# Optimization experiments

Measured on AMD Instinct MI355X. Metric: run time of the kernel, lower is better.

Reference implementation:

```python
import jax, jax.numpy as jnp
import numpy as np

B, DIN, DOUT, GRID_SIZE, SPLINE_ORDER, N_LAYERS = 4096, 1024, 1024, 8, 3, 2
COEFFS = GRID_SIZE + SPLINE_ORDER  # 11


def _kaiming_uniform(key, shape, fan_in):
    # torch nn.init.kaiming_uniform_ default: a=0 -> gain=sqrt(2), bound=sqrt(3)*gain/sqrt(fan_in)
    bound = float(np.sqrt(6.0 / fan_in))
    return jax.random.uniform(key, shape, jnp.float32, -bound, bound)


def setup_inputs() -> dict:
    key = jax.random.key(0)
    ks = jax.random.split(key, 1 + 3 * N_LAYERS)
    x = jax.random.normal(ks[0], (B, DIN), dtype=jnp.float32)
    # knot grid: arange(-so, gs+so+1)*h + lo, h=(hi-lo)/gs  -> shape [GRID_SIZE+2*SPLINE_ORDER+1]
    h = 2.0 / GRID_SIZE
    grid = jnp.arange(-SPLINE_ORDER, GRID_SIZE + SPLINE_ORDER + 1, dtype=jnp.float32) * h - 1.0
    base_w, spline_w, scaler = [], [], []
    for i in range(N_LAYERS):
        base_w.append(_kaiming_uniform(ks[1 + 3 * i], (DOUT, DIN), DIN))
        spline_w.append(_kaiming_uniform(ks[2 + 3 * i], (DOUT, DIN, COEFFS), DIN * COEFFS))
        scaler.append(_kaiming_uniform(ks[3 + 3 * i], (DOUT, DIN), DIN))
    return {
        "x": x,
        "base_w": jnp.stack(base_w),      # [L, DOUT, DIN]
        "spline_w": jnp.stack(spline_w),  # [L, DOUT, DIN, COEFFS]
        "scaler": jnp.stack(scaler),      # [L, DOUT, DIN]
        "grid": grid,                      # [G]
        "spline_order": SPLINE_ORDER,
    }


def b_splines(x, grid, spline_order):
    # x: (B, DIN) -> bases: (B, DIN, COEFFS) via Cox-de Boor recursion
    x = x[..., None]  # (B, DIN, 1)
    bases = ((x >= grid[:-1]) & (x < grid[1:])).astype(x.dtype)  # order-0 indicators
    for k in range(1, spline_order + 1):
        left = (x - grid[: -(k + 1)]) / (grid[k:-1] - grid[: -(k + 1)])
        right = (grid[k + 1:] - x) / (grid[k + 1:] - grid[1:-k])
        bases = left * bases[..., :-1] + right * bases[..., 1:]
    return bases


def reference(x, base_w, spline_w, scaler, grid, spline_order):
    so = int(spline_order)
    n_layers = base_w.shape[0]
    for i in range(n_layers):
        x = jax.nn.silu(x)                                  # base_activation applied before both branches
        base_out = x @ base_w[i].T                          # (B, DOUT)
        bs = b_splines(x, grid, so)                         # (B, DIN, COEFFS)
        w = spline_w[i] * scaler[i][..., None]              # (DOUT, DIN, COEFFS)
        spline_out = jnp.einsum("bic,oic->bo", bs, w)      # == F.linear on flattened (DIN*COEFFS)
        x = base_out + spline_out
    return x
```

## Files before the change

### kernel.cpp

```cpp
#include <hip/hip_runtime.h>
#include <stdint.h>

#define BATCH 4096
#define DIN 1024
#define DOUT 1024
#define NC 11
#define KD 12288
#define NKNOTS 15

typedef __bf16 bf16x8 __attribute__((ext_vector_type(8)));
typedef float f32x4 __attribute__((ext_vector_type(4)));

__device__ __forceinline__ unsigned short f2bf(float f) {
    unsigned int u = __float_as_uint(f);
    unsigned int r = (u + 0x7FFFu + ((u >> 16) & 1u)) >> 16;
    return (unsigned short)r;
}

__global__ __launch_bounds__(256) void build_A(
    const float* __restrict__ x, const float* __restrict__ P, int np,
    const float* __restrict__ grid, unsigned short* __restrict__ A) {
    __shared__ __align__(16) unsigned short lbs[256 * NC];
    const int tid = threadIdx.x;
    const int b  = blockIdx.x >> 2;
    const int i0 = (blockIdx.x & 3) * 256;
    const int i  = i0 + tid;

    float g[NKNOTS];
#pragma unroll
    for (int j = 0; j < NKNOTS; ++j) g[j] = grid[j];

    float xv = x[(size_t)b * DIN + i];
    for (int p = 0; p < np; ++p)
        xv += P[(size_t)p * BATCH * DIN + (size_t)b * DIN + i];
    const float s = xv / (1.f + __expf(-xv));

    float bs[14];
#pragma unroll
    for (int c = 0; c < 14; ++c) bs[c] = (s >= g[c] && s < g[c + 1]) ? 1.f : 0.f;
#pragma unroll
    for (int k = 1; k <= 3; ++k) {
        const float inv = (k == 1) ? 4.f : (k == 2) ? 2.f : (4.f / 3.f);
#pragma unroll
        for (int c = 0; c < 14 - k; ++c) {
            float left  = (s - g[c]) * inv;
            float right = (g[c + k + 1] - s) * inv;
            bs[c] = left * bs[c] + right * bs[c + 1];
        }
    }

    A[(size_t)b * KD + i] = f2bf(s);
#pragma unroll
    for (int c = 0; c < NC; ++c) lbs[tid * NC + c] = f2bf(bs[c]);
    __syncthreads();

    const uint4* src = (const uint4*)lbs;
    uint4* dst = (uint4*)(A + (size_t)b * KD + DIN + (size_t)i0 * NC);
    for (int j = tid; j < 352; j += 256) dst[j] = src[j];
}

__global__ __launch_bounds__(256) void build_W(
    const float* __restrict__ base_w, const float* __restrict__ spline_w,
    const float* __restrict__ scaler, unsigned short* __restrict__ W) {
    __shared__ __align__(16) unsigned short lw[256 * NC];
    const int tid = threadIdx.x;
    const int o  = blockIdx.x >> 2;
    const int i0 = (blockIdx.x & 3) * 256;
    const int i  = i0 + tid;
    const size_t oi = (size_t)o * DIN + i;

    const float sc = scaler[oi];
    W[(size_t)o * KD + i] = f2bf(base_w[oi]);
    const float* sw = spline_w + oi * NC;
#pragma unroll
    for (int c = 0; c < NC; ++c) lw[tid * NC + c] = f2bf(sw[c] * sc);
    __syncthreads();

    const uint4* src = (const uint4*)lw;
    uint4* dst = (uint4*)(W + (size_t)o * KD + DIN + (size_t)i0 * NC);
    for (int j = tid; j < 352; j += 256) dst[j] = src[j];
}

#define BM 256
#define BN 256
#define BK 64

#define LOADAF(AF, BASE)                                                       \
    _Pragma("unroll")                                                          \
    for (int fm = 0; fm < 4; ++fm)                                             \
        _Pragma("unroll")                                                      \
        for (int ks = 0; ks < 2; ++ks)                                         \
            AF[fm][ks] = *(const bf16x8*)&(BASE)[(wm * 64 + fm * 16 + rof) * 64 + \
                                                 (((ks * 4 + kcol) ^ xr) * 8)];

#define LOADBF(BF, BASE)                                                       \
    _Pragma("unroll")                                                          \
    for (int fn = 0; fn < 2; ++fn)                                             \
        _Pragma("unroll")                                                      \
        for (int ks = 0; ks < 2; ++ks)                                         \
            BF[fn][ks] = *(const bf16x8*)&(BASE)[(wn * 32 + fn * 16 + rof) * 64 + \
                                                 (((ks * 4 + kcol) ^ xr) * 8)];

#define MFMA16(AF, BF, RO, CO)                                                 \
    __builtin_amdgcn_s_setprio(1);                                             \
    _Pragma("unroll")                                                          \
    for (int ks = 0; ks < 2; ++ks)                                             \
        _Pragma("unroll")                                                      \
        for (int fm = 0; fm < 4; ++fm)                                         \
            _Pragma("unroll")                                                  \
            for (int fn = 0; fn < 2; ++fn)                                     \
                acc[(RO) + fm][(CO) + fn] =                                    \
                    __builtin_amdgcn_mfma_f32_16x16x32_bf16(                   \
                        AF[fm][ks], BF[fn][ks], acc[(RO) + fm][(CO) + fn], 0, 0, 0); \
    __builtin_amdgcn_s_setprio(0);

#define SBAR  __builtin_amdgcn_s_barrier()
#define SCHED __builtin_amdgcn_sched_barrier(0)

__global__ __launch_bounds__(512, 2) void gemm_kan(
    const unsigned short* __restrict__ A,
    const unsigned short* __restrict__ W,
    float* __restrict__ C, float* __restrict__ Part,
    int kspl, int ktper) {
    __shared__ unsigned short As[2 * 2 * 8192];
    __shared__ unsigned short Bs[2 * 2 * 8192];

    const int tid  = threadIdx.x;
    const int wave = tid >> 6;
    const int lane = tid & 63;
    const int per = 16 * kspl;
    const int n0  = (blockIdx.x / per) * BN;
    const int r   = blockIdx.x % per;
    const int ksp = r % kspl;
    const int m0  = (r / kspl) * BM;
    const int wm = wave >> 2;
    const int wn = wave & 3;

    const int srow = lane >> 3;
    const int scol = 8 * ((lane & 7) ^ (lane >> 3));
    const int kbase = ksp * ktper * BK;

    f32x4 acc[8][4];
#pragma unroll
    for (int a = 0; a < 8; ++a)
#pragma unroll
        for (int b = 0; b < 4; ++b) acc[a][b] = (f32x4){0.f, 0.f, 0.f, 0.f};

    auto stageA = [&](int buf, int h, int kt) {
        const int kk = kbase + kt * BK + scol;
#pragma unroll
        for (int c = 0; c < 2; ++c) {
            const int chunk = wave * 2 + c;
            const unsigned short* ga =
                A + (size_t)(m0 + h * 128 + chunk * 8 + srow) * KD + kk;
            __builtin_amdgcn_global_load_lds(
                (const __attribute__((address_space(1))) unsigned int*)ga,
                (__attribute__((address_space(3))) unsigned int*)
                    &As[buf * 16384 + h * 8192 + chunk * 512], 16, 0, 0);
        }
    };
    auto stageB = [&](int buf, int h, int kt) {
        const int kk = kbase + kt * BK + scol;
#pragma unroll
        for (int c = 0; c < 2; ++c) {
            const int chunk = wave * 2 + c;
            const unsigned short* gb =
                W + (size_t)(n0 + h * 128 + chunk * 8 + srow) * KD + kk;
            __builtin_amdgcn_global_load_lds(
                (const __attribute__((address_space(1))) unsigned int*)gb,
                (__attribute__((address_space(3))) unsigned int*)
                    &Bs[buf * 16384 + h * 8192 + chunk * 512], 16, 0, 0);
        }
    };

    stageB(0, 0, 0); stageB(0, 1, 0); stageA(0, 0, 0); stageA(0, 1, 0);
    asm volatile("s_waitcnt vmcnt(2)" ::: "memory");
    SBAR;

    const int rof  = lane & 15;
    const int xr   = lane & 7;
    const int kcol = lane >> 4;

    bf16x8 af[4][2], b0[2][2], b1[2][2];

    for (int t = 0; t < ktper; ++t) {
        const int cur = t & 1;
        const int nxt = cur ^ 1;
        const bool pf = (t + 1 < ktper);
        const unsigned short* Ab = &As[cur * 16384];
        const unsigned short* Bb = &Bs[cur * 16384];

        LOADAF(af, Ab);
        LOADBF(b0, Bb);
        if (pf) stageB(nxt, 0, t + 1);
        asm volatile("s_waitcnt lgkmcnt(8)" ::: "memory");
        SBAR;
        asm volatile("s_waitcnt lgkmcnt(0)" ::: "memory");
        SCHED;
        MFMA16(af, b0, 0, 0);
        SCHED;
        SBAR;

        LOADBF(b1, Bb + 8192);
        if (pf) stageB(nxt, 1, t + 1);
        SBAR;
        asm volatile("s_waitcnt lgkmcnt(0)" ::: "memory");
        SCHED;
        MFMA16(af, b1, 0, 2);
        SCHED;
        if (pf) { asm volatile("s_waitcnt vmcnt(4)" ::: "memory"); }
        else    { asm volatile("s_waitcnt vmcnt(0)" ::: "memory"); }
        SBAR;

        LOADAF(af, Ab + 8192);
        if (pf) stageA(nxt, 0, t + 1);
        SBAR;
        asm volatile("s_waitcnt lgkmcnt(0)" ::: "memory");
        SCHED;
        MFMA16(af, b1, 4, 2);
        SCHED;
        SBAR;

        if (pf) stageA(nxt, 1, t + 1);
        SBAR;
        SCHED;
        MFMA16(af, b0, 4, 0);
        SCHED;
        if (pf) { asm volatile("s_waitcnt vmcnt(2)" ::: "memory"); }
        SBAR;
    }

    float* Cp = (ksp == 0) ? C : (Part + (size_t)(ksp - 1) * BATCH * DOUT);
    const int crow = (lane >> 4) * 4;
    const int ccol = lane & 15;
#pragma unroll
    for (int H = 0; H < 2; ++H)
#pragma unroll
        for (int fm = 0; fm < 4; ++fm)
#pragma unroll
            for (int F = 0; F < 2; ++F)
#pragma unroll
                for (int fn = 0; fn < 2; ++fn) {
                    const int row = m0 + H * 128 + wm * 64 + fm * 16 + crow;
                    const int col = n0 + F * 128 + wn * 32 + fn * 16 + ccol;
#pragma unroll
                    for (int rr = 0; rr < 4; ++rr)
                        Cp[(size_t)(row + rr) * DOUT + col] =
                            acc[H * 4 + fm][F * 2 + fn][rr];
                }
}

__global__ __launch_bounds__(256) void reduce_add(
    const float* __restrict__ P, float* __restrict__ X, int np) {
    const size_t i = ((size_t)blockIdx.x * 256 + threadIdx.x) * 4;
    f32x4 a = *(const f32x4*)(X + i);
    for (int p = 0; p < np; ++p)
        a = a + *(const f32x4*)(P + (size_t)p * BATCH * DOUT + i);
    *(f32x4*)(X + i) = a;
}

extern "C" void kernel_launch(void* const* d_in, const int* in_sizes, int n_in,
                              void* d_out, int out_size, void* d_ws, size_t ws_size,
                              hipStream_t stream) {
    const float* x        = (const float*)d_in[0];
    const float* base_w   = (const float*)d_in[1];
    const float* spline_w = (const float*)d_in[2];
    const float* scaler   = (const float*)d_in[3];
    const float* grid     = (const float*)d_in[4];
    float* out = (float*)d_out;

    char* ws = (char*)d_ws;
    unsigned short* Abf = (unsigned short*)ws;
    unsigned short* Wbf = (unsigned short*)(ws + 100663296);
    float* xtmp = (float*)(ws + 100663296 + 25165824);
    float* Part = (float*)(ws + 100663296 + 25165824 + 16777216);

    const size_t base_need = 100663296u + 25165824u + 16777216u;
    const int kspl = (ws_size >= base_need + 3u * 16777216u) ? 4 : 2;
    const int ktper = (KD / BK) / kspl;

    for (int layer = 0; layer < 2; ++layer) {
        const float* xin = (layer == 0) ? x : xtmp;
        float* xout      = (layer == 0) ? xtmp : out;
        build_W<<<4096, 256, 0, stream>>>(base_w + (size_t)layer * DOUT * DIN,
                                          spline_w + (size_t)layer * DOUT * DIN * NC,
                                          scaler + (size_t)layer * DOUT * DIN, Wbf);
        build_A<<<16384, 256, 0, stream>>>(xin, Part, (layer == 0) ? 0 : kspl - 1,
                                           grid, Abf);
        gemm_kan<<<64 * kspl, 512, 0, stream>>>(Abf, Wbf, xout, Part, kspl, ktper);
    }
    reduce_add<<<BATCH * DOUT / 1024, 256, 0, stream>>>(Part, out, kspl - 1);
}
```

Measured before the change: 293.7 us.

## Replace split-K partial buffers and reduction with atomic adds into output

```diff
diff --git a/kernel.cpp b/kernel.cpp
--- a/kernel.cpp
+++ b/kernel.cpp
@@ -18,8 +18,8 @@
 }
 
 __global__ __launch_bounds__(256) void build_A(
-    const float* __restrict__ x, const float* __restrict__ P, int np,
-    const float* __restrict__ grid, unsigned short* __restrict__ A) {
+    const float* __restrict__ x, const float* __restrict__ grid,
+    unsigned short* __restrict__ A) {
     __shared__ __align__(16) unsigned short lbs[256 * NC];
     const int tid = threadIdx.x;
     const int b  = blockIdx.x >> 2;
@@ -30,10 +30,8 @@
 #pragma unroll
     for (int j = 0; j < NKNOTS; ++j) g[j] = grid[j];
 
-    float xv = x[(size_t)b * DIN + i];
-    for (int p = 0; p < np; ++p)
-        xv += P[(size_t)p * BATCH * DIN + (size_t)b * DIN + i];
-    const float s = xv / (1.f + __expf(-xv));
+    const float xv = x[(size_t)b * DIN + i];
+    const float s  = xv / (1.f + __expf(-xv));
 
     float bs[14];
 #pragma unroll
@@ -84,6 +82,8 @@
 #define BM 256
 #define BN 256
 #define BK 64
+#define KSPL 4
+#define KTPER 48
 
 #define LOADAF(AF, BASE)                                                       \
     _Pragma("unroll")                                                          \
@@ -120,25 +120,24 @@
 __global__ __launch_bounds__(512, 2) void gemm_kan(
     const unsigned short* __restrict__ A,
     const unsigned short* __restrict__ W,
-    float* __restrict__ C, float* __restrict__ Part,
-    int kspl, int ktper) {
+    float* __restrict__ Out) {
     __shared__ unsigned short As[2 * 2 * 8192];
     __shared__ unsigned short Bs[2 * 2 * 8192];
 
     const int tid  = threadIdx.x;
     const int wave = tid >> 6;
     const int lane = tid & 63;
-    const int per = 16 * kspl;
+    const int per = 16 * KSPL;
     const int n0  = (blockIdx.x / per) * BN;
     const int r   = blockIdx.x % per;
-    const int ksp = r % kspl;
-    const int m0  = (r / kspl) * BM;
+    const int ksp = r % KSPL;
+    const int m0  = (r / KSPL) * BM;
     const int wm = wave >> 2;
     const int wn = wave & 3;
 
     const int srow = lane >> 3;
     const int scol = 8 * ((lane & 7) ^ (lane >> 3));
-    const int kbase = ksp * ktper * BK;
+    const int kbase = ksp * KTPER * BK;
 
     f32x4 acc[8][4];
 #pragma unroll
@@ -183,10 +182,10 @@
 
     bf16x8 af[4][2], b0[2][2], b1[2][2];
 
-    for (int t = 0; t < ktper; ++t) {
+    for (int t = 0; t < KTPER; ++t) {
         const int cur = t & 1;
         const int nxt = cur ^ 1;
-        const bool pf = (t + 1 < ktper);
+        const bool pf = (t + 1 < KTPER);
         const unsigned short* Ab = &As[cur * 16384];
         const unsigned short* Bb = &Bs[cur * 16384];
 
@@ -230,7 +229,6 @@
         SBAR;
     }
 
-    float* Cp = (ksp == 0) ? C : (Part + (size_t)(ksp - 1) * BATCH * DOUT);
     const int crow = (lane >> 4) * 4;
     const int ccol = lane & 15;
 #pragma unroll
@@ -245,18 +243,9 @@
                     const int col = n0 + F * 128 + wn * 32 + fn * 16 + ccol;
 #pragma unroll
                     for (int rr = 0; rr < 4; ++rr)
-                        Cp[(size_t)(row + rr) * DOUT + col] =
-                            acc[H * 4 + fm][F * 2 + fn][rr];
+                        unsafeAtomicAdd(&Out[(size_t)(row + rr) * DOUT + col],
+                                        acc[H * 4 + fm][F * 2 + fn][rr]);
                 }
-}
-
-__global__ __launch_bounds__(256) void reduce_add(
-    const float* __restrict__ P, float* __restrict__ X, int np) {
-    const size_t i = ((size_t)blockIdx.x * 256 + threadIdx.x) * 4;
-    f32x4 a = *(const f32x4*)(X + i);
-    for (int p = 0; p < np; ++p)
-        a = a + *(const f32x4*)(P + (size_t)p * BATCH * DOUT + i);
-    *(f32x4*)(X + i) = a;
 }
 
 extern "C" void kernel_launch(void* const* d_in, const int* in_sizes, int n_in,
@@ -273,11 +262,9 @@
     unsigned short* Abf = (unsigned short*)ws;
     unsigned short* Wbf = (unsigned short*)(ws + 100663296);
     float* xtmp = (float*)(ws + 100663296 + 25165824);
-    float* Part = (float*)(ws + 100663296 + 25165824 + 16777216);
-
-    const size_t base_need = 100663296u + 25165824u + 16777216u;
-    const int kspl = (ws_size >= base_need + 3u * 16777216u) ? 4 : 2;
-    const int ktper = (KD / BK) / kspl;
+
+    hipMemsetAsync(xtmp, 0, (size_t)BATCH * DOUT * 4, stream);
+    hipMemsetAsync(out,  0, (size_t)BATCH * DOUT * 4, stream);
 
     for (int layer = 0; layer < 2; ++layer) {
         const float* xin = (layer == 0) ? x : xtmp;
@@ -285,9 +272,7 @@
         build_W<<<4096, 256, 0, stream>>>(base_w + (size_t)layer * DOUT * DIN,
                                           spline_w + (size_t)layer * DOUT * DIN * NC,
                                           scaler + (size_t)layer * DOUT * DIN, Wbf);
-        build_A<<<16384, 256, 0, stream>>>(xin, Part, (layer == 0) ? 0 : kspl - 1,
-                                           grid, Abf);
-        gemm_kan<<<64 * kspl, 512, 0, stream>>>(Abf, Wbf, xout, Part, kspl, ktper);
+        build_A<<<16384, 256, 0, stream>>>(xin, grid, Abf);
+        gemm_kan<<<64 * KSPL, 512, 0, stream>>>(Abf, Wbf, xout);
     }
-    reduce_add<<<BATCH * DOUT / 1024, 256, 0, stream>>>(Part, out, kspl - 1);
-}
+}
```

New measurement: 350.3 us. 1.19x slower.

## Load GEMM B operand directly from global into registers, bypassing LDS

Applied to the files above, without the earlier changes.

```diff
diff --git a/kernel.cpp b/kernel.cpp
--- a/kernel.cpp
+++ b/kernel.cpp
@@ -93,13 +93,15 @@
             AF[fm][ks] = *(const bf16x8*)&(BASE)[(wm * 64 + fm * 16 + rof) * 64 + \
                                                  (((ks * 4 + kcol) ^ xr) * 8)];
 
-#define LOADBF(BF, BASE)                                                       \
+#define LOADB(DST, KT)                                                         \
     _Pragma("unroll")                                                          \
-    for (int fn = 0; fn < 2; ++fn)                                             \
+    for (int F = 0; F < 2; ++F)                                                \
         _Pragma("unroll")                                                      \
-        for (int ks = 0; ks < 2; ++ks)                                         \
-            BF[fn][ks] = *(const bf16x8*)&(BASE)[(wn * 32 + fn * 16 + rof) * 64 + \
-                                                 (((ks * 4 + kcol) ^ xr) * 8)];
+        for (int fn = 0; fn < 2; ++fn)                                         \
+            _Pragma("unroll")                                                  \
+            for (int ks = 0; ks < 2; ++ks)                                     \
+                DST[F][fn][ks] = *(const bf16x8*)(Wbase +                      \
+                    (size_t)(F * 128 + fn * 16) * KD + (KT) * BK + ks * 32);
 
 #define MFMA16(AF, BF, RO, CO)                                                 \
     __builtin_amdgcn_s_setprio(1);                                             \
@@ -123,7 +125,6 @@
     float* __restrict__ C, float* __restrict__ Part,
     int kspl, int ktper) {
     __shared__ unsigned short As[2 * 2 * 8192];
-    __shared__ unsigned short Bs[2 * 2 * 8192];
 
     const int tid  = threadIdx.x;
     const int wave = tid >> 6;
@@ -159,74 +160,49 @@
                     &As[buf * 16384 + h * 8192 + chunk * 512], 16, 0, 0);
         }
     };
-    auto stageB = [&](int buf, int h, int kt) {
-        const int kk = kbase + kt * BK + scol;
-#pragma unroll
-        for (int c = 0; c < 2; ++c) {
-            const int chunk = wave * 2 + c;
-            const unsigned short* gb =
-                W + (size_t)(n0 + h * 128 + chunk * 8 + srow) * KD + kk;
-            __builtin_amdgcn_global_load_lds(
-                (const __attribute__((address_space(1))) unsigned int*)gb,
-                (__attribute__((address_space(3))) unsigned int*)
-                    &Bs[buf * 16384 + h * 8192 + chunk * 512], 16, 0, 0);
-        }
-    };
-
-    stageB(0, 0, 0); stageB(0, 1, 0); stageA(0, 0, 0); stageA(0, 1, 0);
-    asm volatile("s_waitcnt vmcnt(2)" ::: "memory");
-    SBAR;
 
     const int rof  = lane & 15;
     const int xr   = lane & 7;
     const int kcol = lane >> 4;
 
-    bf16x8 af[4][2], b0[2][2], b1[2][2];
+    const unsigned short* Wbase =
+        W + (size_t)(n0 + wn * 32 + rof) * KD + kbase + kcol * 8;
+
+    bf16x8 af[4][2], bfr[2][2][2];
+
+    stageA(0, 0, 0); stageA(0, 1, 0);
+    LOADB(bfr, 0);
+    asm volatile("s_waitcnt vmcnt(10)" ::: "memory");
+    SBAR;
 
     for (int t = 0; t < ktper; ++t) {
         const int cur = t & 1;
         const int nxt = cur ^ 1;
         const bool pf = (t + 1 < ktper);
         const unsigned short* Ab = &As[cur * 16384];
-        const unsigned short* Bb = &Bs[cur * 16384];
 
         LOADAF(af, Ab);
-        LOADBF(b0, Bb);
-        if (pf) stageB(nxt, 0, t + 1);
-        asm volatile("s_waitcnt lgkmcnt(8)" ::: "memory");
-        SBAR;
+        if (pf) stageA(nxt, 0, t + 1);
         asm volatile("s_waitcnt lgkmcnt(0)" ::: "memory");
         SCHED;
-        MFMA16(af, b0, 0, 0);
-        SCHED;
-        SBAR;
-
-        LOADBF(b1, Bb + 8192);
-        if (pf) stageB(nxt, 1, t + 1);
-        SBAR;
-        asm volatile("s_waitcnt lgkmcnt(0)" ::: "memory");
-        SCHED;
-        MFMA16(af, b1, 0, 2);
-        SCHED;
-        if (pf) { asm volatile("s_waitcnt vmcnt(4)" ::: "memory"); }
+        MFMA16(af, bfr[0], 0, 0);
+        MFMA16(af, bfr[1], 0, 2);
+        SCHED;
+        if (pf) { asm volatile("s_waitcnt vmcnt(2)" ::: "memory"); }
         else    { asm volatile("s_waitcnt vmcnt(0)" ::: "memory"); }
         SBAR;
 
         LOADAF(af, Ab + 8192);
-        if (pf) stageA(nxt, 0, t + 1);
-        SBAR;
+        if (pf) stageA(nxt, 1, t + 1);
         asm volatile("s_waitcnt lgkmcnt(0)" ::: "memory");
         SCHED;
-        MFMA16(af, b1, 4, 2);
-        SCHED;
-        SBAR;
-
-        if (pf) stageA(nxt, 1, t + 1);
-        SBAR;
-        SCHED;
-        MFMA16(af, b0, 4, 0);
-        SCHED;
-        if (pf) { asm volatile("s_waitcnt vmcnt(2)" ::: "memory"); }
+        MFMA16(af, bfr[1], 4, 2);
+        MFMA16(af, bfr[0], 4, 0);
+        SCHED;
+        if (pf) {
+            LOADB(bfr, t + 1);
+            asm volatile("s_waitcnt vmcnt(10)" ::: "memory");
+        }
         SBAR;
     }
 
```

Result: slower. 408.8 us (+39.2%).
